# Kernel optimization log

Measured on AMD Instinct MI355X. Metric: run time of the kernel, lower is better.

## Reference

```python
import jax, jax.numpy as jnp
import numpy as np

N_QUBITS = 18
N_TERMS = 16
N_ANC = 4          # ceil(log2(16))
N_LAYERS = 2
BATCH = 8
D = 2 ** N_QUBITS  # data-register dimension
A = 2 ** N_ANC     # ancilla-register dimension


def setup_inputs() -> dict:
    key = jax.random.key(0)
    k1, k2, k3 = jax.random.split(key, 3)
    x = jax.random.normal(k1, (BATCH, D), dtype=jnp.float32)
    ancilla_params = jax.random.normal(k2, (N_LAYERS * (N_ANC + N_ANC - 1),), dtype=jnp.float32)
    unitary_params = jax.random.normal(k3, (N_TERMS, N_QUBITS), dtype=jnp.float32)
    return {"x": x, "ancilla_params": ancilla_params, "unitary_params": unitary_params}


def _ry(vec, theta, wire, n):
    # single-qubit RY on `wire` of an n-qubit real state vector (wire 0 = MSB)
    left, right = 2 ** wire, 2 ** (n - 1 - wire)
    v = vec.reshape(left, 2, right)
    c, s = jnp.cos(theta / 2), jnp.sin(theta / 2)
    return jnp.stack([c * v[:, 0] - s * v[:, 1], s * v[:, 0] + c * v[:, 1]], axis=1).reshape(-1)


def _cry(vec, theta, ctrl, tgt, n):
    # controlled-RY, ctrl < tgt
    mid, right = 2 ** (tgt - ctrl - 1), 2 ** (n - 1 - tgt)
    v = vec.reshape(2 ** ctrl, 2, mid, 2, right)
    c, s = jnp.cos(theta / 2), jnp.sin(theta / 2)
    a0, a1 = v[:, 1, :, 0, :], v[:, 1, :, 1, :]
    new1 = jnp.stack([c * a0 - s * a1, s * a0 + c * a1], axis=2)
    return v.at[:, 1].set(new1).reshape(-1)


def _ancilla_state(ancilla_params):
    vec = jnp.zeros(A, ancilla_params.dtype).at[0].set(1.0)
    p = 0
    for _ in range(N_LAYERS):
        for i in range(N_ANC):
            vec = _ry(vec, ancilla_params[p], i, N_ANC); p += 1
        for i in range(N_ANC - 1):
            vec = _cry(vec, ancilla_params[p], i, i + 1, N_ANC); p += 1
    return vec


def reference(x, ancilla_params, unitary_params):
    B = x.shape[0]
    # ancilla preparation (acts only on ancilla wires -> product state)
    anc = _ancilla_state(ancilla_params)                      # (A,)
    # AmplitudeEmbedding with normalize=True on data wires
    data = x / jnp.linalg.norm(x, axis=-1, keepdims=True)     # (B, D)
    state = anc[None, :, None] * data[:, None, :]             # (B, A, D)
    # Controlled-RY block k applies RY(unitary_params[k, q]) on data qubit q
    # exactly within ancilla block index a == k. Unused blocks get identity (theta=0).
    thetas = jnp.zeros((A, N_QUBITS), x.dtype).at[:N_TERMS].set(unitary_params)
    c, s = jnp.cos(thetas / 2), jnp.sin(thetas / 2)           # (A, nq)
    for q in range(N_QUBITS):
        left = 2 ** q
        right = D // (2 * left)
        st = state.reshape(B, A, left, 2, right)
        a0, a1 = st[:, :, :, 0, :], st[:, :, :, 1, :]
        cq = c[:, q][None, :, None, None]
        sq = s[:, q][None, :, None, None]
        state = jnp.stack([cq * a0 - sq * a1, sq * a0 + cq * a1], axis=3).reshape(B, A, D)
    # PauliZ expectations on the data wires (marginalize ancilla)
    probs = jnp.sum(state * state, axis=1)                    # (B, D)
    exps = []
    for q in range(N_QUBITS):
        left = 2 ** q
        right = D // (2 * left)
        pq = probs.reshape(B, left, 2, right)
        exps.append(jnp.sum(pq[:, :, 0, :], axis=(1, 2)) - jnp.sum(pq[:, :, 1, :], axis=(1, 2)))
    return jnp.stack(exps, axis=-1).astype(jnp.float32)       # (B, n_qubits)
```

## Files before the change

kernel.cpp:

```cpp
#include <hip/hip_runtime.h>
#include <math.h>

#define D_DIM (1 << 18)
#define NB 8
#define NQ 18
#define NACC 37

#define BLOCKS_PER_ROW 64
#define THREADS 256
#define NBLOCKS (NB * BLOCKS_PER_ROW)


__global__ __launch_bounds__(THREADS) void qc_reduce(const float* __restrict__ x,
                                                     float* __restrict__ ws)
{
    const int UROW = D_DIM / 4;
    const int USEG = UROW / BLOCKS_PER_ROW;
    const int ITER = USEG / THREADS;

    int b   = blockIdx.x / BLOCKS_PER_ROW;
    int seg = blockIdx.x % BLOCKS_PER_ROW;
    int t   = threadIdx.x;
    const float4* rowv = (const float4*)(x + (size_t)b * D_DIM);
    int ubase = seg * USEG;

    float S = 0.f;
    float zacc[18];
    float xacc[18];
#pragma unroll
    for (int k = 0; k < 18; ++k) { zacc[k] = 0.f; xacc[k] = 0.f; }

#pragma unroll
    for (int i = 0; i < ITER; ++i) {
        int u = ubase + i * THREADS + t;
        float4 v = rowv[u];
        float vv = v.x*v.x + v.y*v.y + v.z*v.z + v.w*v.w;
        S += vv;

        zacc[0] += (v.x*v.x - v.y*v.y) + (v.z*v.z - v.w*v.w);
        xacc[0] += 2.f*(v.x*v.y + v.z*v.w);
        zacc[1] += (v.x*v.x + v.y*v.y) - (v.z*v.z + v.w*v.w);
        xacc[1] += 2.f*(v.x*v.z + v.y*v.w);

#pragma unroll
        for (int k = 2; k < 8; ++k) {
            int m = 1 << (k - 2);
            float px = __shfl_xor(v.x, m, 64);
            float py = __shfl_xor(v.y, m, 64);
            float pz = __shfl_xor(v.z, m, 64);
            float pw = __shfl_xor(v.w, m, 64);
            xacc[k] += v.x*px + v.y*py + v.z*pz + v.w*pw;
            zacc[k] += ((u >> (k - 2)) & 1) ? -vv : vv;
        }

#pragma unroll
        for (int k = 8; k < 18; ++k) {
            float4 p = rowv[u ^ (1 << (k - 2))];
            xacc[k] += v.x*p.x + v.y*p.y + v.z*p.z + v.w*p.w;
            zacc[k] += ((u >> (k - 2)) & 1) ? -vv : vv;
        }
    }

    float acc[NACC];
    acc[0] = S;
#pragma unroll
    for (int k = 0; k < 18; ++k) { acc[1 + k] = zacc[k]; acc[19 + k] = xacc[k]; }

    __shared__ float red[4][NACC];
    int lane = t & 63, w = t >> 6;
#pragma unroll
    for (int j = 0; j < NACC; ++j) {
        float v = acc[j];
#pragma unroll
        for (int off = 32; off; off >>= 1) v += __shfl_down(v, off, 64);
        if (lane == 0) red[w][j] = v;
    }
    __syncthreads();
    if (t < NACC) {
        ws[blockIdx.x * NACC + t] = red[0][t] + red[1][t] + red[2][t] + red[3][t];
    }
}

__global__ __launch_bounds__(256) void qc_finalize(const float* __restrict__ ap,
                                                   const float* __restrict__ up,
                                                   const float* __restrict__ ws,
                                                   float* __restrict__ out)
{
    __shared__ float anc2[16];
    __shared__ double tot[NB][NACC];

    if (threadIdx.x == 0) {
        float vec[16];
        for (int i = 0; i < 16; ++i) vec[i] = 0.f;
        vec[0] = 1.f;
        int p = 0;
        for (int layer = 0; layer < 2; ++layer) {
            for (int i = 0; i < 4; ++i) {
                float th = ap[p++] * 0.5f;
                float c = cosf(th), s = sinf(th);
                int m = 1 << (3 - i);
                for (int d0 = 0; d0 < 16; ++d0) {
                    if (d0 & m) continue;
                    float a0 = vec[d0], a1 = vec[d0 | m];
                    vec[d0]     = c*a0 - s*a1;
                    vec[d0 | m] = s*a0 + c*a1;
                }
            }
            for (int i = 0; i < 3; ++i) {
                float th = ap[p++] * 0.5f;
                float c = cosf(th), s = sinf(th);
                int mc = 1 << (3 - i), mt = 1 << (2 - i);
                for (int d0 = 0; d0 < 16; ++d0) {
                    if (!(d0 & mc) || (d0 & mt)) continue;
                    float a0 = vec[d0], a1 = vec[d0 | mt];
                    vec[d0]      = c*a0 - s*a1;
                    vec[d0 | mt] = s*a0 + c*a1;
                }
            }
        }
        for (int a = 0; a < 16; ++a) anc2[a] = vec[a] * vec[a];
    }

    for (int idx = threadIdx.x; idx < NB * NACC; idx += blockDim.x) {
        int b = idx / NACC, j = idx % NACC;
        double s = 0.0;
        const float* base = ws + (size_t)b * BLOCKS_PER_ROW * NACC + j;
#pragma unroll 8
        for (int blk = 0; blk < BLOCKS_PER_ROW; ++blk)
            s += (double)base[blk * NACC];
        tot[b][j] = s;
    }
    __syncthreads();

    int idx = threadIdx.x;
    if (idx < NB * NQ) {
        int b = idx / NQ, q = idx % NQ;
        int k = 17 - q;
        float cw = 0.f, sw = 0.f;
        for (int a = 0; a < 16; ++a) {
            float th = up[a * NQ + q];
            cw += anc2[a] * cosf(th);
            sw += anc2[a] * sinf(th);
        }
        double Sd = tot[b][0];
        double Zd = tot[b][1 + k];
        double Xd = tot[b][19 + k];
        out[idx] = (float)(((double)cw * Zd - (double)sw * Xd) / Sd);
    }
}

extern "C" void kernel_launch(void* const* d_in, const int* in_sizes, int n_in,
                              void* d_out, int out_size, void* d_ws, size_t ws_size,
                              hipStream_t stream)
{
    const float* x  = (const float*)d_in[0];
    const float* ap = (const float*)d_in[1];
    const float* up = (const float*)d_in[2];
    float* out = (float*)d_out;
    float* ws = (float*)d_ws;

    qc_reduce<<<NBLOCKS, THREADS, 0, stream>>>(x, ws);
    qc_finalize<<<1, 256, 0, stream>>>(ap, up, ws, out);
}
```

Baseline: 45.10 us.

## Halve partner loads via pair symmetry, double blocks, parallelize ancilla prep

The cross-term reduction for high qubits now loads each partner element only from the half of the pair with the bit clear, then doubles the accumulator, so redundant global reads are dropped. It relies on block, thread and iteration indices mapping to the relevant address bits. Blocks per row double to 128, which gives more parallelism but makes the finalize kernel sum twice as many partials. The serial single-thread ancilla state preparation is replaced with a wavefront-parallel shuffle version.

```diff
diff --git a/kernel.cpp b/kernel.cpp
--- a/kernel.cpp
+++ b/kernel.cpp
@@ -6,35 +6,36 @@
 #define NQ 18
 #define NACC 37
 
-#define BLOCKS_PER_ROW 64
+#define BPR 128
 #define THREADS 256
-#define NBLOCKS (NB * BLOCKS_PER_ROW)
+#define NBLOCKS (NB * BPR)
+#define UROW (D_DIM / 4)
+#define USEG (UROW / BPR)
+#define NITER (USEG / THREADS)
+
+__device__ __forceinline__ float dot4(float4 a, float4 b) {
+    return a.x*b.x + a.y*b.y + a.z*b.z + a.w*b.w;
+}
 
 
 __global__ __launch_bounds__(THREADS) void qc_reduce(const float* __restrict__ x,
                                                      float* __restrict__ ws)
 {
-    const int UROW = D_DIM / 4;
-    const int USEG = UROW / BLOCKS_PER_ROW;
-    const int ITER = USEG / THREADS;
-
-    int b   = blockIdx.x / BLOCKS_PER_ROW;
-    int seg = blockIdx.x % BLOCKS_PER_ROW;
+    int b   = blockIdx.x / BPR;
+    int seg = blockIdx.x % BPR;
     int t   = threadIdx.x;
     const float4* rowv = (const float4*)(x + (size_t)b * D_DIM);
-    int ubase = seg * USEG;
 
     float S = 0.f;
-    float zacc[18];
-    float xacc[18];
+    float zacc[18], xacc[18];
 #pragma unroll
     for (int k = 0; k < 18; ++k) { zacc[k] = 0.f; xacc[k] = 0.f; }
 
 #pragma unroll
-    for (int i = 0; i < ITER; ++i) {
-        int u = ubase + i * THREADS + t;
+    for (int i = 0; i < NITER; ++i) {
+        int u = seg * USEG + i * THREADS + t;
         float4 v = rowv[u];
-        float vv = v.x*v.x + v.y*v.y + v.z*v.z + v.w*v.w;
+        float vv = dot4(v, v);
         S += vv;
 
         zacc[0] += (v.x*v.x - v.y*v.y) + (v.z*v.z - v.w*v.w);
@@ -54,12 +55,23 @@
         }
 
 #pragma unroll
-        for (int k = 8; k < 18; ++k) {
-            float4 p = rowv[u ^ (1 << (k - 2))];
-            xacc[k] += v.x*p.x + v.y*p.y + v.z*p.z + v.w*p.w;
+        for (int k = 8; k < 18; ++k)
             zacc[k] += ((u >> (k - 2)) & 1) ? -vv : vv;
+
+        if (((t >> 6) & 1) == 0) { float4 p = rowv[u ^ 64];  xacc[8] += dot4(v, p); }
+        if (((t >> 7) & 1) == 0) { float4 p = rowv[u ^ 128]; xacc[9] += dot4(v, p); }
+        if (i == 0) { float4 p = rowv[u ^ 256]; xacc[10] += dot4(v, p); }
+#pragma unroll
+        for (int k = 11; k < 18; ++k) {
+            if (((seg >> (k - 11)) & 1) == 0) {
+                float4 p = rowv[u ^ (1 << (k - 2))];
+                xacc[k] += dot4(v, p);
+            }
         }
     }
+
+#pragma unroll
+    for (int k = 8; k < 18; ++k) xacc[k] *= 2.f;
 
     float acc[NACC];
     acc[0] = S;
@@ -76,9 +88,8 @@
         if (lane == 0) red[w][j] = v;
     }
     __syncthreads();
-    if (t < NACC) {
+    if (t < NACC)
         ws[blockIdx.x * NACC + t] = red[0][t] + red[1][t] + red[2][t] + red[3][t];
-    }
 }
 
 __global__ __launch_bounds__(256) void qc_finalize(const float* __restrict__ ap,
@@ -88,55 +99,51 @@
 {
     __shared__ float anc2[16];
     __shared__ double tot[NB][NACC];
+    int t = threadIdx.x;
 
-    if (threadIdx.x == 0) {
-        float vec[16];
-        for (int i = 0; i < 16; ++i) vec[i] = 0.f;
-        vec[0] = 1.f;
+    if (t < 64) {
+        float c = 1.f, s = 0.f;
+        if (t < 14) { float th = ap[t] * 0.5f; c = cosf(th); s = sinf(th); }
+        float v = (t == 0) ? 1.f : 0.f;
         int p = 0;
         for (int layer = 0; layer < 2; ++layer) {
+#pragma unroll
             for (int i = 0; i < 4; ++i) {
-                float th = ap[p++] * 0.5f;
-                float c = cosf(th), s = sinf(th);
+                float cg = __shfl(c, p, 64), sg = __shfl(s, p, 64); ++p;
                 int m = 1 << (3 - i);
-                for (int d0 = 0; d0 < 16; ++d0) {
-                    if (d0 & m) continue;
-                    float a0 = vec[d0], a1 = vec[d0 | m];
-                    vec[d0]     = c*a0 - s*a1;
-                    vec[d0 | m] = s*a0 + c*a1;
-                }
+                float pv = __shfl_xor(v, m, 64);
+                v = (t & m) ? (sg*pv + cg*v) : (cg*v - sg*pv);
             }
+#pragma unroll
             for (int i = 0; i < 3; ++i) {
-                float th = ap[p++] * 0.5f;
-                float c = cosf(th), s = sinf(th);
+                float cg = __shfl(c, p, 64), sg = __shfl(s, p, 64); ++p;
                 int mc = 1 << (3 - i), mt = 1 << (2 - i);
-                for (int d0 = 0; d0 < 16; ++d0) {
-                    if (!(d0 & mc) || (d0 & mt)) continue;
-                    float a0 = vec[d0], a1 = vec[d0 | mt];
-                    vec[d0]      = c*a0 - s*a1;
-                    vec[d0 | mt] = s*a0 + c*a1;
-                }
+                float pv = __shfl_xor(v, mt, 64);
+                if (t & mc) v = (t & mt) ? (sg*pv + cg*v) : (cg*v - sg*pv);
             }
         }
-        for (int a = 0; a < 16; ++a) anc2[a] = vec[a] * vec[a];
-    }
-
-    for (int idx = threadIdx.x; idx < NB * NACC; idx += blockDim.x) {
-        int b = idx / NACC, j = idx % NACC;
-        double s = 0.0;
-        const float* base = ws + (size_t)b * BLOCKS_PER_ROW * NACC + j;
-#pragma unroll 8
-        for (int blk = 0; blk < BLOCKS_PER_ROW; ++blk)
-            s += (double)base[blk * NACC];
-        tot[b][j] = s;
+        if (t < 16) anc2[t] = v * v;
     }
     __syncthreads();
 
-    int idx = threadIdx.x;
-    if (idx < NB * NQ) {
-        int b = idx / NQ, q = idx % NQ;
+    for (int idx = t; idx < NB * NACC; idx += 256) {
+        int b = idx / NACC, j = idx % NACC;
+        const float* base = ws + (size_t)b * BPR * NACC + j;
+        double s0 = 0.0, s1 = 0.0;
+#pragma unroll 4
+        for (int blk = 0; blk < BPR; blk += 2) {
+            s0 += (double)base[(size_t)blk * NACC];
+            s1 += (double)base[(size_t)(blk + 1) * NACC];
+        }
+        tot[b][j] = s0 + s1;
+    }
+    __syncthreads();
+
+    if (t < NB * NQ) {
+        int b = t / NQ, q = t % NQ;
         int k = 17 - q;
         float cw = 0.f, sw = 0.f;
+#pragma unroll
         for (int a = 0; a < 16; ++a) {
             float th = up[a * NQ + q];
             cw += anc2[a] * cosf(th);
@@ -145,7 +152,7 @@
         double Sd = tot[b][0];
         double Zd = tot[b][1 + k];
         double Xd = tot[b][19 + k];
-        out[idx] = (float)(((double)cw * Zd - (double)sw * Xd) / Sd);
+        out[t] = (float)(((double)cw * Zd - (double)sw * Xd) / Sd);
     }
 }
 
```

New measurement: 38.81 us. -13.9%, faster.
